# Optimization experiments

Measured on AMD Instinct MI355X. Metric: run time of the kernel, lower is better.

The kernel has to match this reference:

```python
import jax, jax.numpy as jnp
import numpy as np

# Qwen3-MoE style config
B, S, D = 2, 2048, 2048        # batch, seqlen, hidden_size
E, I, TOPK = 64, 768, 8        # num_experts, moe_intermediate_size, num_experts_per_tok
M = B * S                      # tokens
CAP = 2 * (M * TOPK) // E


def setup_inputs() -> dict:
    key = jax.random.key(0)
    k0, k1, k2, k3, k4 = jax.random.split(key, 5)
    return {
        "x": jax.random.normal(k0, (B, S, D), jnp.float32),
        "router_weight": jax.random.normal(k1, (D, E), jnp.float32) * 0.02,
        "gate_proj": jax.random.normal(k2, (E, D, I), jnp.float32) * 0.02,
        "up_proj": jax.random.normal(k3, (E, D, I), jnp.float32) * 0.02,
        "down_proj": jax.random.normal(k4, (E, I, D), jnp.float32) * 0.02,
    }


def _moe(x, router_weight, gate_proj, up_proj, down_proj):
    b, s, d = x.shape
    xf = x.reshape(-1, d)                                  # [M, d]
    m = xf.shape[0]

    # ---- TokenChoiceTopKRouter: softmax scores, top-k, renormalize ----
    logits = xf @ router_weight                            # [M, E]
    probs = jax.nn.softmax(logits.astype(jnp.float32), axis=-1)
    topw, topi = jax.lax.top_k(probs, TOPK)                # [M, k]
    topw = topw / topw.sum(axis=-1, keepdims=True)         # norm_topk_prob

    flat_e = topi.reshape(-1)                              # [M*k] expert id per assignment
    flat_w = topw.reshape(-1).astype(x.dtype)              # [M*k] routing weight per assignment

    # ---- permute: sort assignments by expert (stable) ----
    order = jnp.argsort(flat_e)                            # [M*k]
    se = flat_e[order]                                     # sorted expert ids
    tok = order // TOPK                                    # source token per sorted assignment
    counts = jax.ops.segment_sum(jnp.ones_like(flat_e), flat_e, num_segments=E)
    starts = jnp.cumsum(counts) - counts                   # exclusive prefix sum
    pos = jnp.arange(m * TOPK) - starts[se]                # slot within expert's buffer
    valid = pos < CAP
    posc = jnp.minimum(pos, CAP - 1)

    # ---- dispatch to padded per-expert buffers [E, CAP, d] ----
    xe = jnp.zeros((E, CAP, d), x.dtype).at[se, pos].set(xf[tok], mode='drop')

    # ---- grouped SwiGLU experts (batched GEMMs) ----
    h = jax.nn.silu(jnp.einsum('ecd,edi->eci', xe, gate_proj)) \
        * jnp.einsum('ecd,edi->eci', xe, up_proj)          # [E, CAP, I]
    ye = jnp.einsum('eci,eid->ecd', h, down_proj)          # [E, CAP, d]

    # ---- unpermute + weighted combine ----
    contrib = jnp.where(valid[:, None], ye[se, posc], 0.0) * flat_w[order][:, None]
    out = jnp.zeros((m, d), x.dtype).at[tok].add(contrib)  # sum over topk per token
    return out.reshape(b, s, d)


def reference(x, router_weight, gate_proj, up_proj, down_proj):
    return _moe(x, router_weight, gate_proj, up_proj, down_proj)
```

## Files before the change

### kernel.cpp

```cpp
#include <hip/hip_runtime.h>
#include <hip/hip_bf16.h>

typedef __attribute__((ext_vector_type(4))) float f32x4;
typedef __attribute__((ext_vector_type(8))) short bf16x8;
typedef unsigned int   u32;
typedef unsigned short u16;

#define D_DIM 2048
#define I_DIM 768
#define NE    64
#define CAP   1024
#define NTOK  4096

__device__ __forceinline__ u32 cvt2(float a, float b) {
  __hip_bfloat162 hh = __float22bfloat162_rn(float2{a, b});
  union { __hip_bfloat162 h; u32 u; } c; c.h = hh; return c.u;
}
__device__ __forceinline__ u16 f2b(float f) {
  __hip_bfloat16 b = __float2bfloat16(f);
  union { __hip_bfloat16 b; u16 u; } c; c.b = b; return c.u;
}
__device__ __forceinline__ void glp16(const void* g, void* l) {
  __builtin_amdgcn_global_load_lds(
      (const __attribute__((address_space(1))) u32*)g,
      (__attribute__((address_space(3))) u32*)l, 16, 0, 0);
}

__global__ __launch_bounds__(256) void k_cvt_x(const float* __restrict__ x,
                                               u16* __restrict__ xb) {
  const size_t i = ((size_t)blockIdx.x * 256 + threadIdx.x) * 8;
  float4 v0 = *(const float4*)(x + i);
  float4 v1 = *(const float4*)(x + i + 4);
  uint4 o;
  o.x = cvt2(v0.x, v0.y); o.y = cvt2(v0.z, v0.w);
  o.z = cvt2(v1.x, v1.y); o.w = cvt2(v1.z, v1.w);
  *(uint4*)(xb + i) = o;
}

__global__ __launch_bounds__(256) void k_router(
    const float* __restrict__ x, const float* __restrict__ rw,
    int* __restrict__ counts, int* __restrict__ slot_token,
    float* __restrict__ slot_w)
{
  const int lane = threadIdx.x & 63;
  const int tok  = blockIdx.x * 4 + (threadIdx.x >> 6);
  const float* xr = x + (size_t)tok * D_DIM;

  float acc = 0.f;
  for (int d0 = 0; d0 < D_DIM; d0 += 64) {
    float xv = xr[d0 + lane];
    #pragma unroll
    for (int j = 0; j < 64; ++j) {
      float xj = __shfl(xv, j, 64);
      acc = fmaf(xj, rw[(size_t)(d0 + j) * NE + lane], acc);
    }
  }

  float v = acc; int vi = lane;
  float wk[8]; int ei[8];
  float mx0 = 0.f, wsum = 0.f;
  #pragma unroll
  for (int k = 0; k < 8; ++k) {
    float mv = v; int mi = vi;
    #pragma unroll
    for (int off = 32; off >= 1; off >>= 1) {
      float ov = __shfl_xor(mv, off, 64);
      int   oi = __shfl_xor(mi, off, 64);
      if (ov > mv || (ov == mv && oi < mi)) { mv = ov; mi = oi; }
    }
    if (k == 0) mx0 = mv;
    float ew = __expf(mv - mx0);
    wk[k] = ew; ei[k] = mi; wsum += ew;
    if (lane == mi) v = -3.4e38f;
  }

  if (lane == 0) {
    float inv = 1.f / wsum;
    #pragma unroll
    for (int k = 0; k < 8; ++k) {
      int ee   = ei[k];
      int slot = atomicAdd(&counts[ee], 1);
      if (slot < CAP) {
        slot_token[ee * CAP + slot] = tok;
        slot_w[ee * CAP + slot]     = wk[k] * inv;
      }
    }
  }
}

__global__ __launch_bounds__(256, 4) void k_mlp1(
    const u16* __restrict__ xb, const float* __restrict__ gate,
    const float* __restrict__ up, const int* __restrict__ counts,
    const int* __restrict__ slot_token, u16* __restrict__ h)
{
  const int i   = blockIdx.x;
  const int xcd = i & 7;
  const int p   = i >> 3;
  const int mt  = p & 7;
  const int pe  = p >> 3;
  const int val = pe * 8 + xcd;
  const int e   = val / 12;
  const int nt  = val % 12;

  int cnt = counts[e]; if (cnt > CAP) cnt = CAP;
  const int m0 = mt * 128;
  if (m0 >= cnt) return;
  const int n0 = nt * 64;

  const int t = threadIdx.x;
  const int lane = t & 63, wv = t >> 6;
  const int li = lane & 15, gq = lane >> 4;
  const int wr = wv >> 1, wc = wv & 1;

  __shared__ u16 As[2][4 * 128 * 8];
  __shared__ u16 Bg[2][4 * 64 * 8];
  __shared__ u16 Bu[2][4 * 64 * 8];

  const int mh  = wv & 1;
  const int kgA = (wv >> 1) * 2;
  const int tok = slot_token[e * CAP + m0 + mh * 64 + lane];
  const u16* xrow = xb + (size_t)tok * D_DIM;

  const float* gb = gate + (size_t)e * D_DIM * I_DIM + n0 + lane;
  const float* ub = up   + (size_t)e * D_DIM * I_DIM + n0 + lane;

  f32x4 ag[4][2], au[4][2];
  #pragma unroll
  for (int m = 0; m < 4; ++m)
    #pragma unroll
    for (int n = 0; n < 2; ++n) {
      f32x4 z = {0.f, 0.f, 0.f, 0.f};
      ag[m][n] = z; au[m][n] = z;
    }

  float gv[8], uv[8];

  glp16(xrow + (kgA    ) * 8, &As[0][((kgA    ) * 128 + mh * 64) * 8]);
  glp16(xrow + (kgA + 1) * 8, &As[0][((kgA + 1) * 128 + mh * 64) * 8]);
  #pragma unroll
  for (int j = 0; j < 8; ++j) {
    gv[j] = gb[(size_t)(wv * 8 + j) * I_DIM];
    uv[j] = ub[(size_t)(wv * 8 + j) * I_DIM];
  }
  {
    uint4 og, ou;
    og.x = cvt2(gv[0], gv[1]); og.y = cvt2(gv[2], gv[3]);
    og.z = cvt2(gv[4], gv[5]); og.w = cvt2(gv[6], gv[7]);
    ou.x = cvt2(uv[0], uv[1]); ou.y = cvt2(uv[2], uv[3]);
    ou.z = cvt2(uv[4], uv[5]); ou.w = cvt2(uv[6], uv[7]);
    *(uint4*)&Bg[0][(wv * 64 + lane) * 8] = og;
    *(uint4*)&Bu[0][(wv * 64 + lane) * 8] = ou;
  }
  __syncthreads();

  int buf = 0;
  for (int kk = 0; kk < D_DIM; kk += 32) {
    const bool more = (kk + 32) < D_DIM;
    if (more) {
      glp16(xrow + kk + 32 + (kgA    ) * 8, &As[buf ^ 1][((kgA    ) * 128 + mh * 64) * 8]);
      glp16(xrow + kk + 32 + (kgA + 1) * 8, &As[buf ^ 1][((kgA + 1) * 128 + mh * 64) * 8]);
      #pragma unroll
      for (int j = 0; j < 8; ++j) {
        gv[j] = gb[(size_t)(kk + 32 + wv * 8 + j) * I_DIM];
        uv[j] = ub[(size_t)(kk + 32 + wv * 8 + j) * I_DIM];
      }
    }

    {
      bf16x8 a0 = *(const bf16x8*)&As[buf][(gq * 128 + wr * 64 +      li) * 8];
      bf16x8 a1 = *(const bf16x8*)&As[buf][(gq * 128 + wr * 64 + 16 + li) * 8];
      bf16x8 a2 = *(const bf16x8*)&As[buf][(gq * 128 + wr * 64 + 32 + li) * 8];
      bf16x8 a3 = *(const bf16x8*)&As[buf][(gq * 128 + wr * 64 + 48 + li) * 8];
      bf16x8 g0 = *(const bf16x8*)&Bg[buf][(gq * 64 + wc * 32 +      li) * 8];
      bf16x8 g1 = *(const bf16x8*)&Bg[buf][(gq * 64 + wc * 32 + 16 + li) * 8];
      bf16x8 u0 = *(const bf16x8*)&Bu[buf][(gq * 64 + wc * 32 +      li) * 8];
      bf16x8 u1 = *(const bf16x8*)&Bu[buf][(gq * 64 + wc * 32 + 16 + li) * 8];
      ag[0][0] = __builtin_amdgcn_mfma_f32_16x16x32_bf16(a0, g0, ag[0][0], 0, 0, 0);
      ag[1][0] = __builtin_amdgcn_mfma_f32_16x16x32_bf16(a1, g0, ag[1][0], 0, 0, 0);
      ag[2][0] = __builtin_amdgcn_mfma_f32_16x16x32_bf16(a2, g0, ag[2][0], 0, 0, 0);
      ag[3][0] = __builtin_amdgcn_mfma_f32_16x16x32_bf16(a3, g0, ag[3][0], 0, 0, 0);
      ag[0][1] = __builtin_amdgcn_mfma_f32_16x16x32_bf16(a0, g1, ag[0][1], 0, 0, 0);
      ag[1][1] = __builtin_amdgcn_mfma_f32_16x16x32_bf16(a1, g1, ag[1][1], 0, 0, 0);
      ag[2][1] = __builtin_amdgcn_mfma_f32_16x16x32_bf16(a2, g1, ag[2][1], 0, 0, 0);
      ag[3][1] = __builtin_amdgcn_mfma_f32_16x16x32_bf16(a3, g1, ag[3][1], 0, 0, 0);
      au[0][0] = __builtin_amdgcn_mfma_f32_16x16x32_bf16(a0, u0, au[0][0], 0, 0, 0);
      au[1][0] = __builtin_amdgcn_mfma_f32_16x16x32_bf16(a1, u0, au[1][0], 0, 0, 0);
      au[2][0] = __builtin_amdgcn_mfma_f32_16x16x32_bf16(a2, u0, au[2][0], 0, 0, 0);
      au[3][0] = __builtin_amdgcn_mfma_f32_16x16x32_bf16(a3, u0, au[3][0], 0, 0, 0);
      au[0][1] = __builtin_amdgcn_mfma_f32_16x16x32_bf16(a0, u1, au[0][1], 0, 0, 0);
      au[1][1] = __builtin_amdgcn_mfma_f32_16x16x32_bf16(a1, u1, au[1][1], 0, 0, 0);
      au[2][1] = __builtin_amdgcn_mfma_f32_16x16x32_bf16(a2, u1, au[2][1], 0, 0, 0);
      au[3][1] = __builtin_amdgcn_mfma_f32_16x16x32_bf16(a3, u1, au[3][1], 0, 0, 0);
    }

    if (more) {
      uint4 og, ou;
      og.x = cvt2(gv[0], gv[1]); og.y = cvt2(gv[2], gv[3]);
      og.z = cvt2(gv[4], gv[5]); og.w = cvt2(gv[6], gv[7]);
      ou.x = cvt2(uv[0], uv[1]); ou.y = cvt2(uv[2], uv[3]);
      ou.z = cvt2(uv[4], uv[5]); ou.w = cvt2(uv[6], uv[7]);
      *(uint4*)&Bg[buf ^ 1][(wv * 64 + lane) * 8] = og;
      *(uint4*)&Bu[buf ^ 1][(wv * 64 + lane) * 8] = ou;
    }
    __syncthreads();
    buf ^= 1;
  }

  #pragma unroll
  for (int mf = 0; mf < 4; ++mf) {
    #pragma unroll
    for (int j = 0; j < 4; ++j) {
      const int slot = m0 + wr * 64 + mf * 16 + gq * 4 + j;
      u16* hr = h + (size_t)(e * CAP + slot) * I_DIM + n0 + wc * 32 + li;
      #pragma unroll
      for (int nf = 0; nf < 2; ++nf) {
        float gg = ag[mf][nf][j];
        float uu = au[mf][nf][j];
        hr[nf * 16] = f2b(gg * uu / (1.f + __expf(-gg)));
      }
    }
  }
}

__global__ __launch_bounds__(256, 4) void k_mlp2(
    const u16* __restrict__ h, const float* __restrict__ down,
    const int* __restrict__ counts, const int* __restrict__ slot_token,
    const float* __restrict__ slot_w, float* __restrict__ out)
{
  const int i   = blockIdx.x;
  const int xcd = i & 7;
  const int p   = i >> 3;
  const int mt  = p & 7;
  const int pe  = p >> 3;
  const int val = pe * 8 + xcd;
  const int e   = val >> 4;
  const int nt  = val & 15;

  int cnt = counts[e]; if (cnt > CAP) cnt = CAP;
  const int m0 = mt * 128;
  if (m0 >= cnt) return;
  const int n0 = nt * 128;

  const int t = threadIdx.x;
  const int lane = t & 63, wv = t >> 6;
  const int li = lane & 15, gq = lane >> 4;
  const int wm = (wv >> 1) * 64, wn = (wv & 1) * 64;

  __shared__ u16 As[2][4 * 128 * 8];
  __shared__ u16 Bt[2][4 * 128 * 8];

  const int mh  = wv & 1;
  const int kgA = (wv >> 1) * 2;
  const u16* hrow = h + (size_t)(e * CAP + m0 + mh * 64 + lane) * I_DIM;

  const int nB  = t & 127;
  const int kgB = (t >> 7) * 2;
  const float* db = down + (size_t)e * I_DIM * D_DIM + n0 + nB;

  f32x4 acc[4][4];
  #pragma unroll
  for (int m = 0; m < 4; ++m)
    #pragma unroll
    for (int n = 0; n < 4; ++n) { f32x4 z = {0.f,0.f,0.f,0.f}; acc[m][n] = z; }

  float dv[2][8];

  glp16(hrow + (kgA    ) * 8, &As[0][((kgA    ) * 128 + mh * 64) * 8]);
  glp16(hrow + (kgA + 1) * 8, &As[0][((kgA + 1) * 128 + mh * 64) * 8]);
  #pragma unroll
  for (int c = 0; c < 2; ++c)
    #pragma unroll
    for (int j = 0; j < 8; ++j)
      dv[c][j] = db[(size_t)((kgB + c) * 8 + j) * D_DIM];
  #pragma unroll
  for (int c = 0; c < 2; ++c) {
    uint4 o;
    o.x = cvt2(dv[c][0], dv[c][1]); o.y = cvt2(dv[c][2], dv[c][3]);
    o.z = cvt2(dv[c][4], dv[c][5]); o.w = cvt2(dv[c][6], dv[c][7]);
    *(uint4*)&Bt[0][((kgB + c) * 128 + nB) * 8] = o;
  }
  __syncthreads();

  int buf = 0;
  for (int kk = 0; kk < I_DIM; kk += 32) {
    const bool more = (kk + 32) < I_DIM;
    if (more) {
      glp16(hrow + kk + 32 + (kgA    ) * 8, &As[buf ^ 1][((kgA    ) * 128 + mh * 64) * 8]);
      glp16(hrow + kk + 32 + (kgA + 1) * 8, &As[buf ^ 1][((kgA + 1) * 128 + mh * 64) * 8]);
      #pragma unroll
      for (int c = 0; c < 2; ++c)
        #pragma unroll
        for (int j = 0; j < 8; ++j)
          dv[c][j] = db[(size_t)(kk + 32 + (kgB + c) * 8 + j) * D_DIM];
    }

    {
      bf16x8 a[4], b[4];
      #pragma unroll
      for (int mf = 0; mf < 4; ++mf)
        a[mf] = *(const bf16x8*)&As[buf][(gq * 128 + wm + mf * 16 + li) * 8];
      #pragma unroll
      for (int nf = 0; nf < 4; ++nf)
        b[nf] = *(const bf16x8*)&Bt[buf][(gq * 128 + wn + nf * 16 + li) * 8];
      #pragma unroll
      for (int mf = 0; mf < 4; ++mf)
        #pragma unroll
        for (int nf = 0; nf < 4; ++nf)
          acc[mf][nf] = __builtin_amdgcn_mfma_f32_16x16x32_bf16(a[mf], b[nf], acc[mf][nf], 0, 0, 0);
    }

    if (more) {
      #pragma unroll
      for (int c = 0; c < 2; ++c) {
        uint4 o;
        o.x = cvt2(dv[c][0], dv[c][1]); o.y = cvt2(dv[c][2], dv[c][3]);
        o.z = cvt2(dv[c][4], dv[c][5]); o.w = cvt2(dv[c][6], dv[c][7]);
        *(uint4*)&Bt[buf ^ 1][((kgB + c) * 128 + nB) * 8] = o;
      }
    }
    __syncthreads();
    buf ^= 1;
  }

  #pragma unroll
  for (int mf = 0; mf < 4; ++mf) {
    #pragma unroll
    for (int j = 0; j < 4; ++j) {
      const int slot = m0 + wm + mf * 16 + gq * 4 + j;
      if (slot < cnt) {
        const int   tk  = slot_token[e * CAP + slot];
        const float wgt = slot_w[e * CAP + slot];
        float* orow = out + (size_t)tk * D_DIM + n0 + wn + li;
        #pragma unroll
        for (int nf = 0; nf < 4; ++nf)
          atomicAdd(&orow[nf * 16], wgt * acc[mf][nf][j]);
      }
    }
  }
}

extern "C" void kernel_launch(void* const* d_in, const int* in_sizes, int n_in,
                              void* d_out, int out_size, void* d_ws, size_t ws_size,
                              hipStream_t stream) {
  const float* x    = (const float*)d_in[0];
  const float* rw   = (const float*)d_in[1];
  const float* gate = (const float*)d_in[2];
  const float* up   = (const float*)d_in[3];
  const float* down = (const float*)d_in[4];
  float* out = (float*)d_out;

  char* ws = (char*)d_ws;
  int*   counts     = (int*)ws;
  int*   slot_token = (int*)(ws + 1024);
  float* slot_w     = (float*)(ws + 1024 + (size_t)NE * CAP * 4);
  u16*   xb         = (u16*)(ws + 1024 + (size_t)NE * CAP * 8);
  u16*   h          = (u16*)(ws + 1024 + (size_t)NE * CAP * 8
                                  + (size_t)NTOK * D_DIM * 2);

  hipMemsetAsync(counts, 0, NE * sizeof(int), stream);
  hipMemsetAsync(slot_token, 0, (size_t)NE * CAP * sizeof(int), stream);
  hipMemsetAsync(out, 0, (size_t)out_size * sizeof(float), stream);

  k_cvt_x <<<dim3((NTOK * D_DIM) / (256 * 8)), 256, 0, stream>>>(x, xb);
  k_router<<<dim3(NTOK / 4),                   256, 0, stream>>>(x, rw, counts, slot_token, slot_w);
  k_mlp1  <<<dim3(6144),                       256, 0, stream>>>(xb, gate, up, counts, slot_token, h);
  k_mlp2  <<<dim3(8192),                       256, 0, stream>>>(h, down, counts, slot_token, slot_w, out);
}
```

Measured before the change: 1.373 ms.

## Pre-transpose expert weights to bf16 and stream them into LDS with async loads

Adds a transpose-and-convert kernel that rewrites the gate, up and down weights into K-contiguous bf16 copies in workspace every call. The expert GEMM kernels then load B tiles with global_load_lds, the same path the A tiles use, replacing strided fp32 register loads and in-loop conversion. The aim is to cut per-tile register pressure, conversion ALU work and uncoalesced weight reads in the main loops. In exchange it adds a full extra read and write pass over roughly 1.2 GB of fp32 weights per call, and it needs a large workspace or it falls back to the old kernels.

```diff
diff --git a/kernel.cpp b/kernel.cpp
--- a/kernel.cpp
+++ b/kernel.cpp
@@ -37,6 +37,44 @@
   *(uint4*)(xb + i) = o;
 }
 
+__global__ __launch_bounds__(256) void k_cvt_t(const float* __restrict__ in,
+                                               u16* __restrict__ outp,
+                                               int R, int C) {
+  const int e  = blockIdx.z;
+  const int c0 = blockIdx.x * 64;
+  const int r0 = blockIdx.y * 64;
+  const float* ip = in + (size_t)e * R * C;
+  u16* op = outp + (size_t)e * R * C;
+
+  __shared__ u16 T[64][72];
+  const int t  = threadIdx.x;
+  const int rr = t >> 4;
+  const int cc = (t & 15) * 4;
+  #pragma unroll
+  for (int it = 0; it < 4; ++it) {
+    const int r = rr + it * 16;
+    float4 v = *(const float4*)(ip + (size_t)(r0 + r) * C + c0 + cc);
+    T[cc + 0][r] = f2b(v.x);
+    T[cc + 1][r] = f2b(v.y);
+    T[cc + 2][r] = f2b(v.z);
+    T[cc + 3][r] = f2b(v.w);
+  }
+  __syncthreads();
+  const int cw = t >> 3;
+  const int r8 = (t & 7) * 8;
+  #pragma unroll
+  for (int jt = 0; jt < 2; ++jt) {
+    const int c = cw + jt * 32;
+    const u16* s = &T[c][r8];
+    uint4 o;
+    o.x = (u32)s[0] | ((u32)s[1] << 16);
+    o.y = (u32)s[2] | ((u32)s[3] << 16);
+    o.z = (u32)s[4] | ((u32)s[5] << 16);
+    o.w = (u32)s[6] | ((u32)s[7] << 16);
+    *(uint4*)(op + (size_t)(c0 + c) * R + r0 + r8) = o;
+  }
+}
+
 __global__ __launch_bounds__(256) void k_router(
     const float* __restrict__ x, const float* __restrict__ rw,
     int* __restrict__ counts, int* __restrict__ slot_token,
@@ -88,9 +126,10 @@
   }
 }
 
+
 __global__ __launch_bounds__(256, 4) void k_mlp1(
-    const u16* __restrict__ xb, const float* __restrict__ gate,
-    const float* __restrict__ up, const int* __restrict__ counts,
+    const u16* __restrict__ xb, const u16* __restrict__ gT,
+    const u16* __restrict__ uT, const int* __restrict__ counts,
     const int* __restrict__ slot_token, u16* __restrict__ h)
 {
   const int i   = blockIdx.x;
@@ -121,8 +160,11 @@
   const int tok = slot_token[e * CAP + m0 + mh * 64 + lane];
   const u16* xrow = xb + (size_t)tok * D_DIM;
 
-  const float* gb = gate + (size_t)e * D_DIM * I_DIM + n0 + lane;
-  const float* ub = up   + (size_t)e * D_DIM * I_DIM + n0 + lane;
+  const u16* wTb = ((wv >> 1) ? uT : gT) + (size_t)e * D_DIM * I_DIM
+                   + (size_t)(n0 + lane) * D_DIM;
+  u16* Bm0 = (wv >> 1) ? &Bu[0][0] : &Bg[0][0];
+  u16* Bm1 = (wv >> 1) ? &Bu[1][0] : &Bg[1][0];
+  const int kgB = (wv & 1) * 2;
 
   f32x4 ag[4][2], au[4][2];
   #pragma unroll
@@ -133,37 +175,23 @@
       ag[m][n] = z; au[m][n] = z;
     }
 
-  float gv[8], uv[8];
-
-  glp16(xrow + (kgA    ) * 8, &As[0][((kgA    ) * 128 + mh * 64) * 8]);
+  glp16(xrow + kgA * 8,       &As[0][(kgA * 128 + mh * 64) * 8]);
   glp16(xrow + (kgA + 1) * 8, &As[0][((kgA + 1) * 128 + mh * 64) * 8]);
-  #pragma unroll
-  for (int j = 0; j < 8; ++j) {
-    gv[j] = gb[(size_t)(wv * 8 + j) * I_DIM];
-    uv[j] = ub[(size_t)(wv * 8 + j) * I_DIM];
-  }
-  {
-    uint4 og, ou;
-    og.x = cvt2(gv[0], gv[1]); og.y = cvt2(gv[2], gv[3]);
-    og.z = cvt2(gv[4], gv[5]); og.w = cvt2(gv[6], gv[7]);
-    ou.x = cvt2(uv[0], uv[1]); ou.y = cvt2(uv[2], uv[3]);
-    ou.z = cvt2(uv[4], uv[5]); ou.w = cvt2(uv[6], uv[7]);
-    *(uint4*)&Bg[0][(wv * 64 + lane) * 8] = og;
-    *(uint4*)&Bu[0][(wv * 64 + lane) * 8] = ou;
-  }
+  glp16(wTb + kgB * 8,        Bm0 + (kgB * 64) * 8);
+  glp16(wTb + (kgB + 1) * 8,  Bm0 + ((kgB + 1) * 64) * 8);
   __syncthreads();
 
   int buf = 0;
   for (int kk = 0; kk < D_DIM; kk += 32) {
-    const bool more = (kk + 32) < D_DIM;
-    if (more) {
-      glp16(xrow + kk + 32 + (kgA    ) * 8, &As[buf ^ 1][((kgA    ) * 128 + mh * 64) * 8]);
-      glp16(xrow + kk + 32 + (kgA + 1) * 8, &As[buf ^ 1][((kgA + 1) * 128 + mh * 64) * 8]);
-      #pragma unroll
-      for (int j = 0; j < 8; ++j) {
-        gv[j] = gb[(size_t)(kk + 32 + wv * 8 + j) * I_DIM];
-        uv[j] = ub[(size_t)(kk + 32 + wv * 8 + j) * I_DIM];
-      }
+    if (kk + 32 < D_DIM) {
+      const u16* xp = xrow + kk + 32;
+      const u16* wp = wTb + kk + 32;
+      u16* An = &As[buf ^ 1][0];
+      u16* Bn = buf ? Bm0 : Bm1;
+      glp16(xp + kgA * 8,       An + (kgA * 128 + mh * 64) * 8);
+      glp16(xp + (kgA + 1) * 8, An + ((kgA + 1) * 128 + mh * 64) * 8);
+      glp16(wp + kgB * 8,       Bn + (kgB * 64) * 8);
+      glp16(wp + (kgB + 1) * 8, Bn + ((kgB + 1) * 64) * 8);
     }
 
     {
@@ -192,7 +220,225 @@
       au[2][1] = __builtin_amdgcn_mfma_f32_16x16x32_bf16(a2, u1, au[2][1], 0, 0, 0);
       au[3][1] = __builtin_amdgcn_mfma_f32_16x16x32_bf16(a3, u1, au[3][1], 0, 0, 0);
     }
-
+    __syncthreads();
+    buf ^= 1;
+  }
+
+  #pragma unroll
+  for (int mf = 0; mf < 4; ++mf) {
+    #pragma unroll
+    for (int j = 0; j < 4; ++j) {
+      const int slot = m0 + wr * 64 + mf * 16 + gq * 4 + j;
+      u16* hr = h + (size_t)(e * CAP + slot) * I_DIM + n0 + wc * 32 + li;
+      #pragma unroll
+      for (int nf = 0; nf < 2; ++nf) {
+        float gg = ag[mf][nf][j];
+        float uu = au[mf][nf][j];
+        hr[nf * 16] = f2b(gg * uu / (1.f + __expf(-gg)));
+      }
+    }
+  }
+}
+
+__global__ __launch_bounds__(256, 4) void k_mlp2(
+    const u16* __restrict__ h, const u16* __restrict__ dT,
+    const int* __restrict__ counts, const int* __restrict__ slot_token,
+    const float* __restrict__ slot_w, float* __restrict__ out)
+{
+  const int i   = blockIdx.x;
+  const int xcd = i & 7;
+  const int p   = i >> 3;
+  const int mt  = p & 7;
+  const int pe  = p >> 3;
+  const int val = pe * 8 + xcd;
+  const int e   = val >> 4;
+  const int nt  = val & 15;
+
+  int cnt = counts[e]; if (cnt > CAP) cnt = CAP;
+  const int m0 = mt * 128;
+  if (m0 >= cnt) return;
+  const int n0 = nt * 128;
+
+  const int t = threadIdx.x;
+  const int lane = t & 63, wv = t >> 6;
+  const int li = lane & 15, gq = lane >> 4;
+  const int wm = (wv >> 1) * 64, wn = (wv & 1) * 64;
+
+  __shared__ u16 As[2][4 * 128 * 8];
+  __shared__ u16 Bt[2][4 * 128 * 8];
+
+  const int mh  = wv & 1;
+  const int kgA = (wv >> 1) * 2;
+  const u16* hrow = h + (size_t)(e * CAP + m0 + mh * 64 + lane) * I_DIM;
+
+  const int nh   = wv & 1;
+  const int kgB0 = wv >> 1;
+  const u16* drow = dT + (size_t)e * I_DIM * D_DIM
+                    + (size_t)(n0 + nh * 64 + lane) * I_DIM;
+
+  f32x4 acc[4][4];
+  #pragma unroll
+  for (int m = 0; m < 4; ++m)
+    #pragma unroll
+    for (int n = 0; n < 4; ++n) { f32x4 z = {0.f,0.f,0.f,0.f}; acc[m][n] = z; }
+
+  glp16(hrow + kgA * 8,          &As[0][(kgA * 128 + mh * 64) * 8]);
+  glp16(hrow + (kgA + 1) * 8,    &As[0][((kgA + 1) * 128 + mh * 64) * 8]);
+  glp16(drow + kgB0 * 8,         &Bt[0][(kgB0 * 128 + nh * 64) * 8]);
+  glp16(drow + (kgB0 + 2) * 8,   &Bt[0][((kgB0 + 2) * 128 + nh * 64) * 8]);
+  __syncthreads();
+
+  int buf = 0;
+  for (int kk = 0; kk < I_DIM; kk += 32) {
+    if (kk + 32 < I_DIM) {
+      const u16* hp = hrow + kk + 32;
+      const u16* dp = drow + kk + 32;
+      u16* An = &As[buf ^ 1][0];
+      u16* Bn = &Bt[buf ^ 1][0];
+      glp16(hp + kgA * 8,        An + (kgA * 128 + mh * 64) * 8);
+      glp16(hp + (kgA + 1) * 8,  An + ((kgA + 1) * 128 + mh * 64) * 8);
+      glp16(dp + kgB0 * 8,       Bn + (kgB0 * 128 + nh * 64) * 8);
+      glp16(dp + (kgB0 + 2) * 8, Bn + ((kgB0 + 2) * 128 + nh * 64) * 8);
+    }
+
+    {
+      bf16x8 a[4], b[4];
+      #pragma unroll
+      for (int mf = 0; mf < 4; ++mf)
+        a[mf] = *(const bf16x8*)&As[buf][(gq * 128 + wm + mf * 16 + li) * 8];
+      #pragma unroll
+      for (int nf = 0; nf < 4; ++nf)
+        b[nf] = *(const bf16x8*)&Bt[buf][(gq * 128 + wn + nf * 16 + li) * 8];
+      #pragma unroll
+      for (int mf = 0; mf < 4; ++mf)
+        #pragma unroll
+        for (int nf = 0; nf < 4; ++nf)
+          acc[mf][nf] = __builtin_amdgcn_mfma_f32_16x16x32_bf16(a[mf], b[nf], acc[mf][nf], 0, 0, 0);
+    }
+    __syncthreads();
+    buf ^= 1;
+  }
+
+  #pragma unroll
+  for (int mf = 0; mf < 4; ++mf) {
+    #pragma unroll
+    for (int j = 0; j < 4; ++j) {
+      const int slot = m0 + wm + mf * 16 + gq * 4 + j;
+      if (slot < cnt) {
+        const int   tk  = slot_token[e * CAP + slot];
+        const float wgt = slot_w[e * CAP + slot];
+        float* orow = out + (size_t)tk * D_DIM + n0 + wn + li;
+        #pragma unroll
+        for (int nf = 0; nf < 4; ++nf)
+          atomicAdd(&orow[nf * 16], wgt * acc[mf][nf][j]);
+      }
+    }
+  }
+}
+
+
+__global__ __launch_bounds__(256, 4) void k_mlp1f(
+    const u16* __restrict__ xb, const float* __restrict__ gate,
+    const float* __restrict__ up, const int* __restrict__ counts,
+    const int* __restrict__ slot_token, u16* __restrict__ h)
+{
+  const int i   = blockIdx.x;
+  const int xcd = i & 7;
+  const int p   = i >> 3;
+  const int mt  = p & 7;
+  const int pe  = p >> 3;
+  const int val = pe * 8 + xcd;
+  const int e   = val / 12;
+  const int nt  = val % 12;
+
+  int cnt = counts[e]; if (cnt > CAP) cnt = CAP;
+  const int m0 = mt * 128;
+  if (m0 >= cnt) return;
+  const int n0 = nt * 64;
+
+  const int t = threadIdx.x;
+  const int lane = t & 63, wv = t >> 6;
+  const int li = lane & 15, gq = lane >> 4;
+  const int wr = wv >> 1, wc = wv & 1;
+
+  __shared__ u16 As[2][4 * 128 * 8];
+  __shared__ u16 Bg[2][4 * 64 * 8];
+  __shared__ u16 Bu[2][4 * 64 * 8];
+
+  const int mh  = wv & 1;
+  const int kgA = (wv >> 1) * 2;
+  const int tok = slot_token[e * CAP + m0 + mh * 64 + lane];
+  const u16* xrow = xb + (size_t)tok * D_DIM;
+
+  const float* gb = gate + (size_t)e * D_DIM * I_DIM + n0 + lane;
+  const float* ub = up   + (size_t)e * D_DIM * I_DIM + n0 + lane;
+
+  f32x4 ag[4][2], au[4][2];
+  #pragma unroll
+  for (int m = 0; m < 4; ++m)
+    #pragma unroll
+    for (int n = 0; n < 2; ++n) {
+      f32x4 z = {0.f, 0.f, 0.f, 0.f};
+      ag[m][n] = z; au[m][n] = z;
+    }
+
+  float gv[8], uv[8];
+  glp16(xrow + kgA * 8,       &As[0][(kgA * 128 + mh * 64) * 8]);
+  glp16(xrow + (kgA + 1) * 8, &As[0][((kgA + 1) * 128 + mh * 64) * 8]);
+  #pragma unroll
+  for (int j = 0; j < 8; ++j) {
+    gv[j] = gb[(size_t)(wv * 8 + j) * I_DIM];
+    uv[j] = ub[(size_t)(wv * 8 + j) * I_DIM];
+  }
+  {
+    uint4 og, ou;
+    og.x = cvt2(gv[0], gv[1]); og.y = cvt2(gv[2], gv[3]);
+    og.z = cvt2(gv[4], gv[5]); og.w = cvt2(gv[6], gv[7]);
+    ou.x = cvt2(uv[0], uv[1]); ou.y = cvt2(uv[2], uv[3]);
+    ou.z = cvt2(uv[4], uv[5]); ou.w = cvt2(uv[6], uv[7]);
+    *(uint4*)&Bg[0][(wv * 64 + lane) * 8] = og;
+    *(uint4*)&Bu[0][(wv * 64 + lane) * 8] = ou;
+  }
+  __syncthreads();
+
+  int buf = 0;
+  for (int kk = 0; kk < D_DIM; kk += 32) {
+    const bool more = (kk + 32) < D_DIM;
+    if (more) {
+      glp16(xrow + kk + 32 + kgA * 8,       &As[buf ^ 1][(kgA * 128 + mh * 64) * 8]);
+      glp16(xrow + kk + 32 + (kgA + 1) * 8, &As[buf ^ 1][((kgA + 1) * 128 + mh * 64) * 8]);
+      #pragma unroll
+      for (int j = 0; j < 8; ++j) {
+        gv[j] = gb[(size_t)(kk + 32 + wv * 8 + j) * I_DIM];
+        uv[j] = ub[(size_t)(kk + 32 + wv * 8 + j) * I_DIM];
+      }
+    }
+    {
+      bf16x8 a0 = *(const bf16x8*)&As[buf][(gq * 128 + wr * 64 +      li) * 8];
+      bf16x8 a1 = *(const bf16x8*)&As[buf][(gq * 128 + wr * 64 + 16 + li) * 8];
+      bf16x8 a2 = *(const bf16x8*)&As[buf][(gq * 128 + wr * 64 + 32 + li) * 8];
+      bf16x8 a3 = *(const bf16x8*)&As[buf][(gq * 128 + wr * 64 + 48 + li) * 8];
+      bf16x8 g0 = *(const bf16x8*)&Bg[buf][(gq * 64 + wc * 32 +      li) * 8];
+      bf16x8 g1 = *(const bf16x8*)&Bg[buf][(gq * 64 + wc * 32 + 16 + li) * 8];
+      bf16x8 u0 = *(const bf16x8*)&Bu[buf][(gq * 64 + wc * 32 +      li) * 8];
+      bf16x8 u1 = *(const bf16x8*)&Bu[buf][(gq * 64 + wc * 32 + 16 + li) * 8];
+      ag[0][0] = __builtin_amdgcn_mfma_f32_16x16x32_bf16(a0, g0, ag[0][0], 0, 0, 0);
+      ag[1][0] = __builtin_amdgcn_mfma_f32_16x16x32_bf16(a1, g0, ag[1][0], 0, 0, 0);
+      ag[2][0] = __builtin_amdgcn_mfma_f32_16x16x32_bf16(a2, g0, ag[2][0], 0, 0, 0);
+      ag[3][0] = __builtin_amdgcn_mfma_f32_16x16x32_bf16(a3, g0, ag[3][0], 0, 0, 0);
+      ag[0][1] = __builtin_amdgcn_mfma_f32_16x16x32_bf16(a0, g1, ag[0][1], 0, 0, 0);
+      ag[1][1] = __builtin_amdgcn_mfma_f32_16x16x32_bf16(a1, g1, ag[1][1], 0, 0, 0);
+      ag[2][1] = __builtin_amdgcn_mfma_f32_16x16x32_bf16(a2, g1, ag[2][1], 0, 0, 0);
+      ag[3][1] = __builtin_amdgcn_mfma_f32_16x16x32_bf16(a3, g1, ag[3][1], 0, 0, 0);
+      au[0][0] = __builtin_amdgcn_mfma_f32_16x16x32_bf16(a0, u0, au[0][0], 0, 0, 0);
+      au[1][0] = __builtin_amdgcn_mfma_f32_16x16x32_bf16(a1, u0, au[1][0], 0, 0, 0);
+      au[2][0] = __builtin_amdgcn_mfma_f32_16x16x32_bf16(a2, u0, au[2][0], 0, 0, 0);
+      au[3][0] = __builtin_amdgcn_mfma_f32_16x16x32_bf16(a3, u0, au[3][0], 0, 0, 0);
+      au[0][1] = __builtin_amdgcn_mfma_f32_16x16x32_bf16(a0, u1, au[0][1], 0, 0, 0);
+      au[1][1] = __builtin_amdgcn_mfma_f32_16x16x32_bf16(a1, u1, au[1][1], 0, 0, 0);
+      au[2][1] = __builtin_amdgcn_mfma_f32_16x16x32_bf16(a2, u1, au[2][1], 0, 0, 0);
+      au[3][1] = __builtin_amdgcn_mfma_f32_16x16x32_bf16(a3, u1, au[3][1], 0, 0, 0);
+    }
     if (more) {
       uint4 og, ou;
       og.x = cvt2(gv[0], gv[1]); og.y = cvt2(gv[2], gv[3]);
@@ -222,7 +468,7 @@
   }
 }
 
-__global__ __launch_bounds__(256, 4) void k_mlp2(
+__global__ __launch_bounds__(256, 4) void k_mlp2f(
     const u16* __restrict__ h, const float* __restrict__ down,
     const int* __restrict__ counts, const int* __restrict__ slot_token,
     const float* __restrict__ slot_w, float* __restrict__ out)
@@ -264,8 +510,7 @@
     for (int n = 0; n < 4; ++n) { f32x4 z = {0.f,0.f,0.f,0.f}; acc[m][n] = z; }
 
   float dv[2][8];
-
-  glp16(hrow + (kgA    ) * 8, &As[0][((kgA    ) * 128 + mh * 64) * 8]);
+  glp16(hrow + kgA * 8,       &As[0][(kgA * 128 + mh * 64) * 8]);
   glp16(hrow + (kgA + 1) * 8, &As[0][((kgA + 1) * 128 + mh * 64) * 8]);
   #pragma unroll
   for (int c = 0; c < 2; ++c)
@@ -285,7 +530,7 @@
   for (int kk = 0; kk < I_DIM; kk += 32) {
     const bool more = (kk + 32) < I_DIM;
     if (more) {
-      glp16(hrow + kk + 32 + (kgA    ) * 8, &As[buf ^ 1][((kgA    ) * 128 + mh * 64) * 8]);
+      glp16(hrow + kk + 32 + kgA * 8,       &As[buf ^ 1][(kgA * 128 + mh * 64) * 8]);
       glp16(hrow + kk + 32 + (kgA + 1) * 8, &As[buf ^ 1][((kgA + 1) * 128 + mh * 64) * 8]);
       #pragma unroll
       for (int c = 0; c < 2; ++c)
@@ -293,7 +538,6 @@
         for (int j = 0; j < 8; ++j)
           dv[c][j] = db[(size_t)(kk + 32 + (kgB + c) * 8 + j) * D_DIM];
     }
-
     {
       bf16x8 a[4], b[4];
       #pragma unroll
@@ -308,7 +552,6 @@
         for (int nf = 0; nf < 4; ++nf)
           acc[mf][nf] = __builtin_amdgcn_mfma_f32_16x16x32_bf16(a[mf], b[nf], acc[mf][nf], 0, 0, 0);
     }
-
     if (more) {
       #pragma unroll
       for (int c = 0; c < 2; ++c) {
@@ -352,10 +595,15 @@
   char* ws = (char*)d_ws;
   int*   counts     = (int*)ws;
   int*   slot_token = (int*)(ws + 1024);
-  float* slot_w     = (float*)(ws + 1024 + (size_t)NE * CAP * 4);
-  u16*   xb         = (u16*)(ws + 1024 + (size_t)NE * CAP * 8);
-  u16*   h          = (u16*)(ws + 1024 + (size_t)NE * CAP * 8
-                                  + (size_t)NTOK * D_DIM * 2);
+  float* slot_w     = (float*)(ws + 1024 + 262144);
+  u16*   xb         = (u16*)(ws + 1024 + 524288);
+  u16*   h          = (u16*)(ws + 1024 + 524288 + 16777216);
+  const size_t base = 1024 + 524288 + 16777216 + 100663296ull;
+  const size_t WSLAB = 201326592ull;
+  u16* gT = (u16*)(ws + base);
+  u16* uT = (u16*)(ws + base + WSLAB);
+  u16* dT = (u16*)(ws + base + 2 * WSLAB);
+  const bool wb = ws_size >= base + 3 * WSLAB;
 
   hipMemsetAsync(counts, 0, NE * sizeof(int), stream);
   hipMemsetAsync(slot_token, 0, (size_t)NE * CAP * sizeof(int), stream);
@@ -363,6 +611,15 @@
 
   k_cvt_x <<<dim3((NTOK * D_DIM) / (256 * 8)), 256, 0, stream>>>(x, xb);
   k_router<<<dim3(NTOK / 4),                   256, 0, stream>>>(x, rw, counts, slot_token, slot_w);
-  k_mlp1  <<<dim3(6144),                       256, 0, stream>>>(xb, gate, up, counts, slot_token, h);
-  k_mlp2  <<<dim3(8192),                       256, 0, stream>>>(h, down, counts, slot_token, slot_w, out);
-}
+
+  if (wb) {
+    k_cvt_t<<<dim3(12, 32, NE), 256, 0, stream>>>(gate, gT, D_DIM, I_DIM);
+    k_cvt_t<<<dim3(12, 32, NE), 256, 0, stream>>>(up,   uT, D_DIM, I_DIM);
+    k_cvt_t<<<dim3(32, 12, NE), 256, 0, stream>>>(down, dT, I_DIM, D_DIM);
+    k_mlp1<<<dim3(6144), 256, 0, stream>>>(xb, gT, uT, counts, slot_token, h);
+    k_mlp2<<<dim3(8192), 256, 0, stream>>>(h, dT, counts, slot_token, slot_w, out);
+  } else {
+    k_mlp1f<<<dim3(6144), 256, 0, stream>>>(xb, gate, up, counts, slot_token, h);
+    k_mlp2f<<<dim3(8192), 256, 0, stream>>>(h, down, counts, slot_token, slot_w, out);
+  }
+}
```

New measurement: 1.732 ms. +26.2%, slower.
